# Optimization experiments

Measured on AMD Instinct MI355X. Metric: run time of the kernel, lower is better.

## Reference

```python
import jax, jax.numpy as jnp
import numpy as np

N_NODES = 50000
N_EDGES = 800000


def _sage_layer(h, src, dst, ew, Ws, Wn, b, activate):
    # DGL SAGEConv, aggregator_type='mean', with edge weights:
    # message m_e = ew_e * h_src ; neigh = mean over incoming edges (divide by in-degree)
    msg = h[src] * ew[:, None]                       # [E, F] irregular gather
    agg = jax.ops.segment_sum(msg, dst, num_segments=N_NODES)
    deg = jax.ops.segment_sum(jnp.ones_like(ew), dst, num_segments=N_NODES)
    h_neigh = agg / jnp.maximum(deg, 1.0)[:, None]   # zero for isolated nodes
    out = h @ Ws + h_neigh @ Wn + b                  # fc_self + fc_neigh + bias
    return jnp.tanh(out) if activate else out


def setup_inputs() -> dict:
    key = jax.random.key(0)
    ks = jax.random.split(key, 12)
    d = 64
    inp = {
        "b_z": jax.random.normal(ks[0], (N_NODES, d), dtype=jnp.float32),
        "edge_src": jax.random.randint(ks[1], (N_EDGES,), 0, N_NODES, dtype=jnp.int32),
        "edge_dst": jax.random.randint(ks[2], (N_EDGES,), 0, N_NODES, dtype=jnp.int32),
        "edge_weight": jax.random.uniform(ks[3], (N_EDGES,), dtype=jnp.float32),
        "Ws0": jax.random.normal(ks[4], (64, 32), dtype=jnp.float32) / np.sqrt(64),
        "Wn0": jax.random.normal(ks[5], (64, 32), dtype=jnp.float32) / np.sqrt(64),
        "b0": jnp.zeros((32,), jnp.float32),
        "Ws1": jax.random.normal(ks[6], (32, 16), dtype=jnp.float32) / np.sqrt(32),
        "Wn1": jax.random.normal(ks[7], (32, 16), dtype=jnp.float32) / np.sqrt(32),
        "b1": jnp.zeros((16,), jnp.float32),
        "Ws2": jax.random.normal(ks[8], (16, 1), dtype=jnp.float32) / np.sqrt(16),
        "Wn2": jax.random.normal(ks[9], (16, 1), dtype=jnp.float32) / np.sqrt(16),
        "b2": jnp.zeros((1,), jnp.float32),
        "b_size": 500,
    }
    return inp


def reference(b_z, edge_src, edge_dst, edge_weight,
              Ws0, Wn0, b0, Ws1, Wn1, b1, Ws2, Wn2, b2, b_size):
    h = _sage_layer(b_z, edge_src, edge_dst, edge_weight, Ws0, Wn0, b0, True)
    h = _sage_layer(h, edge_src, edge_dst, edge_weight, Ws1, Wn1, b1, True)
    h = _sage_layer(h, edge_src, edge_dst, edge_weight, Ws2, Wn2, b2, False)
    x_hat = h.reshape(b_size, -1)
    return x_hat
```

## Files before the change

### kernel.cpp

```cpp
#include <hip/hip_runtime.h>
#include <hip/hip_bf16.h>

#define N_NODES 50000
#define N_EDGES 800000
#define NXCD 8
#define NPX 6250
#define BLK 256
#define CAP 64

#define EW_SCALE (1.0f / 65535.0f)

__device__ inline void unpack8(uint4 g, float* f) {
    f[0] = __uint_as_float(g.x << 16); f[1] = __uint_as_float(g.x & 0xffff0000u);
    f[2] = __uint_as_float(g.y << 16); f[3] = __uint_as_float(g.y & 0xffff0000u);
    f[4] = __uint_as_float(g.z << 16); f[5] = __uint_as_float(g.z & 0xffff0000u);
    f[6] = __uint_as_float(g.w << 16); f[7] = __uint_as_float(g.w & 0xffff0000u);
}
__device__ inline void unpack4(uint2 g, float* f) {
    f[0] = __uint_as_float(g.x << 16); f[1] = __uint_as_float(g.x & 0xffff0000u);
    f[2] = __uint_as_float(g.y << 16); f[3] = __uint_as_float(g.y & 0xffff0000u);
}

__global__ void zero_pack_premul0_kernel(int* __restrict__ counts,
                                         const int* __restrict__ src,
                                         const float* __restrict__ ew,
                                         unsigned int* __restrict__ pay,
                                         const float* __restrict__ b_z,
                                         const float* __restrict__ Wn0,
                                         const float* __restrict__ Ws0,
                                         const float* __restrict__ b0,
                                         __hip_bfloat16* __restrict__ hW0,
                                         float* __restrict__ hSelf0, int N, int E) {
    int tid = threadIdx.x;
    for (int i = blockIdx.x * BLK + tid; i < N; i += gridDim.x * BLK) counts[i] = 0;
    for (int e = blockIdx.x * BLK + tid; e < E; e += gridDim.x * BLK) {
        unsigned int q = __float2uint_rn(ew[e] * 65535.0f);
        pay[e] = (q << 16) | (unsigned int)src[e];
    }

    __shared__ float sWn[64 * 32];
    __shared__ float sWs[64 * 32];
    __shared__ float sb[32];
    __shared__ float sh[8 * 65];
    for (int i = tid; i < 64 * 32; i += BLK) { sWn[i] = Wn0[i]; sWs[i] = Ws0[i]; }
    if (tid < 32) sb[tid] = b0[tid];
    const int nch = (N + 7) / 8;
    int r = tid >> 5, j = tid & 31;
    for (int c = blockIdx.x; c < nch; c += gridDim.x) {
        __syncthreads();
        int nodeBase = c * 8;
        for (int i = tid; i < 8 * 64; i += BLK) {
            int rr = i >> 6, k = i & 63;
            int n = nodeBase + rr;
            sh[rr * 65 + k] = (n < N) ? b_z[(size_t)n * 64 + k] : 0.f;
        }
        __syncthreads();
        int n = nodeBase + r;
        if (n < N) {
            float an = 0.f, as = 0.f;
#pragma unroll
            for (int k = 0; k < 64; ++k) {
                float hk = sh[r * 65 + k];
                an += hk * sWn[k * 32 + j];
                as += hk * sWs[k * 32 + j];
            }
            hW0[(size_t)n * 32 + j] = __float2bfloat16(an);
            hSelf0[(size_t)n * 32 + j] = as + sb[j];
        }
    }
}

__global__ void fill_kernel(const int* __restrict__ dst,
                            const unsigned int* __restrict__ pay,
                            int* __restrict__ counts,
                            unsigned int* __restrict__ bucket, int E) {
    int xcd = blockIdx.x & (NXCD - 1);
    int s   = blockIdx.x >> 3;
    int nstripes = gridDim.x >> 3;
    int lo = xcd * NPX, hi = lo + NPX;
    for (int e = s * BLK + threadIdx.x; e < E; e += nstripes * BLK) {
        int d = __builtin_nontemporal_load(dst + e);
        if (d >= lo && d < hi) {
            int p = atomicAdd(&counts[d], 1);
            if (p < CAP) bucket[(size_t)d * CAP + p] = __builtin_nontemporal_load(pay + e);
        }
    }
}

__global__ void agg0_kernel(const __hip_bfloat16* __restrict__ hW0,
                            const float* __restrict__ hSelf0,
                            const int* __restrict__ cnts,
                            const unsigned int* __restrict__ bucket,
                            const float* __restrict__ Wn1,
                            const float* __restrict__ Ws1,
                            const float* __restrict__ b1,
                            __hip_bfloat16* __restrict__ hW1,
                            float* __restrict__ hSelf1, int N) {
    __shared__ float sWn[32 * 16];
    __shared__ float sWs[32 * 16];
    __shared__ float sb[16];
    __shared__ float sh2[64 * 33];
    int tid = threadIdx.x;
    for (int i = tid; i < 32 * 16; i += BLK) { sWn[i] = Wn1[i]; sWs[i] = Ws1[i]; }
    if (tid < 16) sb[tid] = b1[tid];

    const uint4* __restrict__ tab = (const uint4*)hW0;
    int nodeBase = blockIdx.x * 64;
    int r = tid >> 2;
    int l = tid & 3;
    int n = nodeBase + r;
    if (n < N) {
        int cnt = cnts[n];
        int cn  = min(cnt, CAP);
        const unsigned int* __restrict__ ep = bucket + (size_t)n * CAP;
        float acc[8];
#pragma unroll
        for (int t = 0; t < 8; ++t) acc[t] = 0.f;
        int k = 0;
        for (; k + 8 <= cn; k += 8) {
            uint4 ev0 = *(const uint4*)(ep + k);
            uint4 ev1 = *(const uint4*)(ep + k + 4);
            unsigned int ee[8] = { ev0.x, ev0.y, ev0.z, ev0.w,
                                   ev1.x, ev1.y, ev1.z, ev1.w };
            uint4 g[8];
            float w[8];
#pragma unroll
            for (int u = 0; u < 8; ++u) {
                g[u] = tab[(size_t)(ee[u] & 0xffffu) * 4 + l];
                w[u] = (float)(ee[u] >> 16) * EW_SCALE;
            }
#pragma unroll
            for (int u = 0; u < 8; ++u) {
                float f[8];
                unpack8(g[u], f);
#pragma unroll
                for (int t = 0; t < 8; ++t) acc[t] += w[u] * f[t];
            }
        }
        for (; k < cn; ++k) {
            unsigned int e = ep[k];
            float w = (float)(e >> 16) * EW_SCALE;
            uint4 g = tab[(size_t)(e & 0xffffu) * 4 + l];
            float f[8];
            unpack8(g, f);
#pragma unroll
            for (int t = 0; t < 8; ++t) acc[t] += w * f[t];
        }
        float invdeg = 1.0f / fmaxf((float)cnt, 1.0f);
        const float4* __restrict__ hs = (const float4*)(hSelf0 + (size_t)n * 32);
        float4 s0 = hs[l * 2], s1 = hs[l * 2 + 1];
        float sf[8] = { s0.x, s0.y, s0.z, s0.w, s1.x, s1.y, s1.z, s1.w };
#pragma unroll
        for (int t = 0; t < 8; ++t)
            sh2[r * 33 + l * 8 + t] = tanhf(acc[t] * invdeg + sf[t]);
    }
    __syncthreads();
    for (int idx = tid; idx < 64 * 16; idx += BLK) {
        int r2 = idx >> 4, j2 = idx & 15;
        int n2 = nodeBase + r2;
        if (n2 < N) {
            float an = 0.f, as = 0.f;
#pragma unroll
            for (int k = 0; k < 32; ++k) {
                float hk = sh2[r2 * 33 + k];
                an += hk * sWn[k * 16 + j2];
                as += hk * sWs[k * 16 + j2];
            }
            hW1[(size_t)n2 * 16 + j2] = __float2bfloat16(an);
            hSelf1[(size_t)n2 * 16 + j2] = as + sb[j2];
        }
    }
}

__global__ void agg1_kernel(const __hip_bfloat16* __restrict__ hW1,
                            const float* __restrict__ hSelf1,
                            const int* __restrict__ cnts,
                            const unsigned int* __restrict__ bucket,
                            const float* __restrict__ Wn2,
                            const float* __restrict__ Ws2,
                            const float* __restrict__ b2,
                            float* __restrict__ hWf,
                            float* __restrict__ hSelf2, int N) {
    int tid = threadIdx.x;
    int r = tid >> 2;
    int l = tid & 3;
    int n = blockIdx.x * 64 + r;
    if (n >= N) return;

    const uint2* __restrict__ tab = (const uint2*)hW1;
    int cnt = cnts[n];
    int cn  = min(cnt, CAP);
    const unsigned int* __restrict__ ep = bucket + (size_t)n * CAP;
    float acc[4];
#pragma unroll
    for (int t = 0; t < 4; ++t) acc[t] = 0.f;
    int k = 0;
    for (; k + 8 <= cn; k += 8) {
        uint4 ev0 = *(const uint4*)(ep + k);
        uint4 ev1 = *(const uint4*)(ep + k + 4);
        unsigned int ee[8] = { ev0.x, ev0.y, ev0.z, ev0.w,
                               ev1.x, ev1.y, ev1.z, ev1.w };
        uint2 g[8];
        float w[8];
#pragma unroll
        for (int u = 0; u < 8; ++u) {
            g[u] = tab[(size_t)(ee[u] & 0xffffu) * 4 + l];
            w[u] = (float)(ee[u] >> 16) * EW_SCALE;
        }
#pragma unroll
        for (int u = 0; u < 8; ++u) {
            float f[4];
            unpack4(g[u], f);
#pragma unroll
            for (int t = 0; t < 4; ++t) acc[t] += w[u] * f[t];
        }
    }
    for (; k < cn; ++k) {
        unsigned int e = ep[k];
        float w = (float)(e >> 16) * EW_SCALE;
        uint2 g = tab[(size_t)(e & 0xffffu) * 4 + l];
        float f[4];
        unpack4(g, f);
#pragma unroll
        for (int t = 0; t < 4; ++t) acc[t] += w * f[t];
    }
    float invdeg = 1.0f / fmaxf((float)cnt, 1.0f);
    const float4* __restrict__ hs = (const float4*)(hSelf1 + (size_t)n * 16);
    float4 sv = hs[l];
    float sf[4] = { sv.x, sv.y, sv.z, sv.w };
    float t2 = 0.f, t3 = 0.f;
#pragma unroll
    for (int t = 0; t < 4; ++t) {
        float hv = tanhf(acc[t] * invdeg + sf[t]);
        t2 += hv * Wn2[l * 4 + t];
        t3 += hv * Ws2[l * 4 + t];
    }
    t2 += __shfl_xor(t2, 1, 4); t2 += __shfl_xor(t2, 2, 4);
    t3 += __shfl_xor(t3, 1, 4); t3 += __shfl_xor(t3, 2, 4);
    if (l == 0) {
        hWf[n] = t2;
        hSelf2[n] = t3 + b2[0];
    }
}

__global__ void agg_final_kernel(const float* __restrict__ hWf,
                                 const float* __restrict__ hSelf2,
                                 const int* __restrict__ cnts,
                                 const unsigned int* __restrict__ bucket,
                                 float* __restrict__ out, int N) {
    int sub = threadIdx.x & 15;
    int r   = threadIdx.x >> 4;
    int n   = blockIdx.x * 16 + r;
    if (n >= N) return;
    int cnt = cnts[n];
    int cn  = min(cnt, CAP);
    const unsigned int* __restrict__ ep = bucket + (size_t)n * CAP;
    float a = 0.f;
    for (int k = sub; k < cn; k += 16) {
        unsigned int e = ep[k];
        a += ((float)(e >> 16) * EW_SCALE) * hWf[e & 0xffffu];
    }
#pragma unroll
    for (int m = 8; m >= 1; m >>= 1) a += __shfl_xor(a, m, 16);
    if (sub == 0) {
        float invdeg = 1.0f / fmaxf((float)cnt, 1.0f);
        out[n] = a * invdeg + hSelf2[n];
    }
}

extern "C" void kernel_launch(void* const* d_in, const int* in_sizes, int n_in,
                              void* d_out, int out_size, void* d_ws, size_t ws_size,
                              hipStream_t stream) {
    const float* b_z = (const float*)d_in[0];
    const int*   src = (const int*)d_in[1];
    const int*   dst = (const int*)d_in[2];
    const float* ew  = (const float*)d_in[3];
    const float* Ws0 = (const float*)d_in[4];
    const float* Wn0 = (const float*)d_in[5];
    const float* b0  = (const float*)d_in[6];
    const float* Ws1 = (const float*)d_in[7];
    const float* Wn1 = (const float*)d_in[8];
    const float* b1  = (const float*)d_in[9];
    const float* Ws2 = (const float*)d_in[10];
    const float* Wn2 = (const float*)d_in[11];
    const float* b2  = (const float*)d_in[12];

    const int N = N_NODES;
    const int E = N_EDGES;
    const int GRID_E = 2048;

    int*          counts = (int*)d_ws;
    unsigned int* pay    = (unsigned int*)(counts + N);
    unsigned int* bucket = pay + E;
    __hip_bfloat16* hW0  = (__hip_bfloat16*)(bucket + (size_t)N * CAP);
    __hip_bfloat16* hW1  = hW0 + (size_t)N * 32;
    float* hWf    = (float*)(hW1 + (size_t)N * 16);
    float* hSelf0 = hWf + N;
    float* hSelf1 = hSelf0 + (size_t)N * 32;
    float* hSelf2 = hSelf1 + (size_t)N * 16;
    float* outp   = (float*)d_out;

    zero_pack_premul0_kernel<<<GRID_E, BLK, 0, stream>>>(
        counts, src, ew, pay, b_z, Wn0, Ws0, b0, hW0, hSelf0, N, E);
    fill_kernel<<<GRID_E, BLK, 0, stream>>>(dst, pay, counts, bucket, E);
    agg0_kernel<<<(N + 63) / 64, BLK, 0, stream>>>(
        hW0, hSelf0, counts, bucket, Wn1, Ws1, b1, hW1, hSelf1, N);
    agg1_kernel<<<(N + 63) / 64, BLK, 0, stream>>>(
        hW1, hSelf1, counts, bucket, Wn2, Ws2, b2, hWf, hSelf2, N);
    agg_final_kernel<<<(N + 15) / 16, BLK, 0, stream>>>(
        hWf, hSelf2, counts, bucket, outp, N);
}
```

Measured before the change: 110.1 us.

## Partition edges by destination XCD range before bucket scatter

Replaces the fill kernel, in which every block scanned all edges and kept only those whose destination fell in its XCD's node range, with two steps. A partition kernel first bins packed edges into per-XCD lists using shared-memory counters and global cursors. A scatter kernel then reads only its own XCD's list. This removes the eightfold redundant read of dst and payload, at the cost of an extra kernel launch, an extra write and read of 8-byte edge records, and a larger workspace.

```diff
diff --git a/kernel.cpp b/kernel.cpp
--- a/kernel.cpp
+++ b/kernel.cpp
@@ -7,6 +7,7 @@
 #define NPX 6250
 #define BLK 256
 #define CAP 64
+#define CHUNK 400
 
 #define EW_SCALE (1.0f / 65535.0f)
 
@@ -21,22 +22,17 @@
     f[2] = __uint_as_float(g.y << 16); f[3] = __uint_as_float(g.y & 0xffff0000u);
 }
 
-__global__ void zero_pack_premul0_kernel(int* __restrict__ counts,
-                                         const int* __restrict__ src,
-                                         const float* __restrict__ ew,
-                                         unsigned int* __restrict__ pay,
-                                         const float* __restrict__ b_z,
-                                         const float* __restrict__ Wn0,
-                                         const float* __restrict__ Ws0,
-                                         const float* __restrict__ b0,
-                                         __hip_bfloat16* __restrict__ hW0,
-                                         float* __restrict__ hSelf0, int N, int E) {
+__global__ void zero_premul0_kernel(int* __restrict__ counts,
+                                    int* __restrict__ cursors,
+                                    const float* __restrict__ b_z,
+                                    const float* __restrict__ Wn0,
+                                    const float* __restrict__ Ws0,
+                                    const float* __restrict__ b0,
+                                    __hip_bfloat16* __restrict__ hW0,
+                                    float* __restrict__ hSelf0, int N) {
     int tid = threadIdx.x;
     for (int i = blockIdx.x * BLK + tid; i < N; i += gridDim.x * BLK) counts[i] = 0;
-    for (int e = blockIdx.x * BLK + tid; e < E; e += gridDim.x * BLK) {
-        unsigned int q = __float2uint_rn(ew[e] * 65535.0f);
-        pay[e] = (q << 16) | (unsigned int)src[e];
-    }
+    if (blockIdx.x == 0 && tid < NXCD) cursors[tid] = 0;
 
     __shared__ float sWn[64 * 32];
     __shared__ float sWs[64 * 32];
@@ -70,20 +66,50 @@
     }
 }
 
-__global__ void fill_kernel(const int* __restrict__ dst,
-                            const unsigned int* __restrict__ pay,
-                            int* __restrict__ counts,
-                            unsigned int* __restrict__ bucket, int E) {
+__global__ void partition_kernel(const int* __restrict__ src,
+                                 const int* __restrict__ dst,
+                                 const float* __restrict__ ew,
+                                 int* __restrict__ cursors,
+                                 uint2* __restrict__ lists, int E) {
+    __shared__ uint2 se[CHUNK];
+    __shared__ int slot[CHUNK];
+    __shared__ int cnt8[NXCD];
+    __shared__ int base8[NXCD];
+    int tid = threadIdx.x;
+    if (tid < NXCD) cnt8[tid] = 0;
+    int beg = blockIdx.x * CHUNK;
+    int m = min(beg + CHUNK, E) - beg;
+    __syncthreads();
+    for (int i = tid; i < m; i += BLK) {
+        int e = beg + i;
+        int d = dst[e];
+        unsigned int q = __float2uint_rn(ew[e] * 65535.0f);
+        se[i] = make_uint2((q << 16) | (unsigned int)src[e], (unsigned int)d);
+        slot[i] = atomicAdd(&cnt8[d / NPX], 1);
+    }
+    __syncthreads();
+    if (tid < NXCD) base8[tid] = atomicAdd(&cursors[tid], cnt8[tid]);
+    __syncthreads();
+    for (int i = tid; i < m; i += BLK) {
+        int x = se[i].y / NPX;
+        lists[(size_t)x * E + base8[x] + slot[i]] = se[i];
+    }
+}
+
+__global__ void scatter_kernel(const uint2* __restrict__ lists,
+                               const int* __restrict__ cursors,
+                               int* __restrict__ counts,
+                               unsigned int* __restrict__ bucket, int E) {
     int xcd = blockIdx.x & (NXCD - 1);
     int s   = blockIdx.x >> 3;
     int nstripes = gridDim.x >> 3;
-    int lo = xcd * NPX, hi = lo + NPX;
-    for (int e = s * BLK + threadIdx.x; e < E; e += nstripes * BLK) {
-        int d = __builtin_nontemporal_load(dst + e);
-        if (d >= lo && d < hi) {
-            int p = atomicAdd(&counts[d], 1);
-            if (p < CAP) bucket[(size_t)d * CAP + p] = __builtin_nontemporal_load(pay + e);
-        }
+    int cnt = cursors[xcd];
+    const uint2* __restrict__ lp = lists + (size_t)xcd * E;
+    for (int i = s * BLK + threadIdx.x; i < cnt; i += nstripes * BLK) {
+        uint2 e = lp[i];
+        int d = (int)e.y;
+        int p = atomicAdd(&counts[d], 1);
+        if (p < CAP) bucket[(size_t)d * CAP + p] = e.x;
     }
 }
 
@@ -288,21 +314,24 @@
     const int N = N_NODES;
     const int E = N_EDGES;
     const int GRID_E = 2048;
-
-    int*          counts = (int*)d_ws;
-    unsigned int* pay    = (unsigned int*)(counts + N);
-    unsigned int* bucket = pay + E;
-    __hip_bfloat16* hW0  = (__hip_bfloat16*)(bucket + (size_t)N * CAP);
-    __hip_bfloat16* hW1  = hW0 + (size_t)N * 32;
+    const int GRID_P = (E + CHUNK - 1) / CHUNK;
+
+    int*          counts  = (int*)d_ws;
+    int*          cursors = counts + N;
+    uint2*        lists   = (uint2*)(cursors + NXCD);
+    unsigned int* bucket  = (unsigned int*)(lists + (size_t)NXCD * E);
+    __hip_bfloat16* hW0   = (__hip_bfloat16*)(bucket + (size_t)N * CAP);
+    __hip_bfloat16* hW1   = hW0 + (size_t)N * 32;
     float* hWf    = (float*)(hW1 + (size_t)N * 16);
     float* hSelf0 = hWf + N;
     float* hSelf1 = hSelf0 + (size_t)N * 32;
     float* hSelf2 = hSelf1 + (size_t)N * 16;
     float* outp   = (float*)d_out;
 
-    zero_pack_premul0_kernel<<<GRID_E, BLK, 0, stream>>>(
-        counts, src, ew, pay, b_z, Wn0, Ws0, b0, hW0, hSelf0, N, E);
-    fill_kernel<<<GRID_E, BLK, 0, stream>>>(dst, pay, counts, bucket, E);
+    zero_premul0_kernel<<<GRID_E, BLK, 0, stream>>>(counts, cursors, b_z,
+                                                    Wn0, Ws0, b0, hW0, hSelf0, N);
+    partition_kernel<<<GRID_P, BLK, 0, stream>>>(src, dst, ew, cursors, lists, E);
+    scatter_kernel<<<GRID_E, BLK, 0, stream>>>(lists, cursors, counts, bucket, E);
     agg0_kernel<<<(N + 63) / 64, BLK, 0, stream>>>(
         hW0, hSelf0, counts, bucket, Wn1, Ws1, b1, hW1, hSelf1, N);
     agg1_kernel<<<(N + 63) / 64, BLK, 0, stream>>>(
```

New measurement: 134.4 us. +22.1%, slower.
